# Performance work log

Hardware: AMD Instinct MI355X
Metric: run time of the kernel (lower is better)

The kernel has to match this reference:

```python
import jax, jax.numpy as jnp
import numpy as np

N = 100000
E = 3200000
NEG_SLOPE = 0.2


def _gat(x, W, a_src, a_dst, b, src, dst, n):
    """PyG-style GATConv (eval mode, self-loops already appended to src/dst)."""
    H, C = a_src.shape
    h = (x @ W).reshape(n, H, C)                       # [N,H,C]
    es = jnp.einsum('nhc,hc->nh', h, a_src)            # per-node src logits
    ed = jnp.einsum('nhc,hc->nh', h, a_dst)
    e = jax.nn.leaky_relu(es[src] + ed[dst], NEG_SLOPE)  # [E,H]
    m = jax.ops.segment_max(e, dst, num_segments=n)    # stable softmax per dst
    ee = jnp.exp(e - m[dst])
    z = jax.ops.segment_sum(ee, dst, num_segments=n)
    alpha = ee / z[dst]                                # softmax over in-edges
    out = jax.ops.segment_sum(h[src] * alpha[:, :, None], dst, num_segments=n)
    return out.reshape(n, H * C) + b


def setup_inputs() -> dict:
    key = jax.random.key(0)
    ks = jax.random.split(key, 25)
    rn = lambda k, s, sc=0.1: jax.random.normal(k, s, dtype=jnp.float32) * sc
    return {
        'x1': rn(ks[0], (N, 8), 1.0),
        'x2': rn(ks[1], (N, 10), 1.0),
        'edge_index': jax.random.randint(ks[2], (2, E), 0, N, dtype=jnp.int32),
        'num_nodes': N,
        'Wq': rn(ks[3], (8, 16)), 'bq': rn(ks[4], (16,)),
        'Wk': rn(ks[5], (10, 16)), 'bk': rn(ks[6], (16,)),
        'Wv': rn(ks[7], (18, 16)), 'bv': rn(ks[8], (16,)),
        'W1': rn(ks[9], (16, 32)), 'a1s': rn(ks[10], (8, 4)), 'a1d': rn(ks[11], (8, 4)), 'b1': rn(ks[12], (32,)),
        'W2': rn(ks[13], (32, 16)), 'a2s': rn(ks[14], (4, 4)), 'a2d': rn(ks[15], (4, 4)), 'b2': rn(ks[16], (16,)),
        'W3': rn(ks[17], (16, 8)), 'a3s': rn(ks[18], (2, 4)), 'a3d': rn(ks[19], (2, 4)), 'b3': rn(ks[20], (8,)),
        'Wl2': rn(ks[21], (8, 1)),
    }


def reference(x1, x2, edge_index, num_nodes, Wq, bq, Wk, bk, Wv, bv,
              W1, a1s, a1d, b1, W2, a2s, a2d, b2, W3, a3s, a3d, b3, Wl2):
    n = num_nodes
    q = x1 @ Wq + bq                                   # [N,16]
    k = x2 @ Wk + bk                                   # [N,16]
    v = jnp.concatenate([x1, x2], axis=1) @ Wv + bv    # [N,16]
    score = jnp.sum(q * k, axis=1)                     # bmm(q[:,None,:], k[:,:,None]).squeeze()
    attw = jax.nn.softmax(score)[:, None]              # softmax over all nodes
    fused = attw * v                                   # [N,16]

    sl = jnp.arange(n, dtype=edge_index.dtype)         # GATConv adds self-loops
    src = jnp.concatenate([edge_index[0], sl])
    dst = jnp.concatenate([edge_index[1], sl])

    h1 = _gat(fused, W1, a1s, a1d, b1, src, dst, n)    # [N,32]
    h2 = _gat(h1, W2, a2s, a2d, b2, src, dst, n)       # [N,16]
    x4 = _gat(h2, W3, a3s, a3d, b3, src, dst, n)       # [N,8]; dropout=identity (eval)

    # Row-normalized adjacency (no self loops), expressed as O(E) segment ops.
    r, c = edge_index[0], edge_index[1]
    deg = jax.ops.segment_sum(jnp.ones_like(r, dtype=x4.dtype), r, num_segments=n)
    inv = jnp.where(deg > 0, 1.0 / deg, 0.0)[:, None]
    R3 = jax.ops.segment_sum(x4[c], r, num_segments=n) * inv  # Adj_norm @ x4
    local = jnp.sum(x4 * R3, axis=1, keepdims=True)    # sum_j Adjn[i,j]*(x4_i . x4_j)
    glob = R3 @ Wl2                                    # lin2 (no bias)
    return local + glob                                # [N,1]
```

## Files before the change

kernel.cpp:

```cpp
#include <hip/hip_runtime.h>

#define TPB 256
#define CAP 9216
#define EPB 4096
#define OFSW 784
#define GBPAD 784

typedef float f32x4 __attribute__((ext_vector_type(4)));
typedef float f32x2 __attribute__((ext_vector_type(2)));

__device__ __forceinline__ float lrelu(float x) { return x > 0.f ? x : 0.2f * x; }

__device__ __forceinline__ unsigned bfr(float x) {
  unsigned u = __float_as_uint(x);
  return (u + 0x7FFFu + ((u >> 16) & 1u)) >> 16;
}
__device__ __forceinline__ unsigned pk(float a, float b) { return bfr(a) | (bfr(b) << 16); }
__device__ __forceinline__ float ubf(unsigned us) { return __uint_as_float(us << 16); }

__global__ void __launch_bounds__(TPB) k_bucket(
    const int* __restrict__ ei, int E, int N,
    unsigned* __restrict__ items2, int* __restrict__ ofs)
{
  __shared__ int hist[1024];
  __shared__ int lofs[1024];
  __shared__ int scan_s[TPB];
  __shared__ unsigned stage[2 * EPB];
  int tid = threadIdx.x;
  for (int i = tid; i < 1024; i += TPB) hist[i] = 0;
  int s0 = blockIdx.x * EPB;
  int nE = min(EPB, E - s0);
  int sv[16], dv[16];
  __syncthreads();
#pragma unroll
  for (int k = 0; k < 4; k++) {
    int li = tid * 4 + k * TPB * 4;
    if (li + 3 < nE) {
      int4 s4 = *(const int4*)(ei + s0 + li);
      int4 d4 = *(const int4*)(ei + E + s0 + li);
      sv[k*4+0] = s4.x; sv[k*4+1] = s4.y; sv[k*4+2] = s4.z; sv[k*4+3] = s4.w;
      dv[k*4+0] = d4.x; dv[k*4+1] = d4.y; dv[k*4+2] = d4.z; dv[k*4+3] = d4.w;
#pragma unroll
      for (int j = 0; j < 4; j++) {
        atomicAdd(&hist[dv[k*4+j] >> 8], 1);
        atomicAdd(&hist[(N + sv[k*4+j]) >> 8], 1);
      }
    } else {
      for (int j = 0; j < 4; j++) {
        if (li + j < nE) {
          sv[k*4+j] = ei[s0 + li + j];
          dv[k*4+j] = ei[E + s0 + li + j];
          atomicAdd(&hist[dv[k*4+j] >> 8], 1);
          atomicAdd(&hist[(N + sv[k*4+j]) >> 8], 1);
        }
      }
    }
  }
  __syncthreads();
  int b0 = tid * 4;
  int c0 = hist[b0], c1 = hist[b0 + 1], c2 = hist[b0 + 2], c3 = hist[b0 + 3];
  int tsum = c0 + c1 + c2 + c3;
  scan_s[tid] = tsum;
  __syncthreads();
#pragma unroll
  for (int o = 1; o < TPB; o <<= 1) {
    int t = (tid >= o) ? scan_s[tid - o] : 0;
    __syncthreads();
    scan_s[tid] += t;
    __syncthreads();
  }
  int run = scan_s[tid] - tsum;
  int cs[4] = {c0, c1, c2, c3};
#pragma unroll
  for (int j = 0; j < 4; j++) {
    int b = b0 + j;
    lofs[b] = run;
    hist[b] = 0;
    run += cs[j];
  }
  __syncthreads();
#pragma unroll
  for (int k = 0; k < 16; k++) {
    int li = tid * 4 + (k >> 2) * TPB * 4 + (k & 3);
    if (li < nE) {
      int s = sv[k], d = dv[k];
      int b1 = d >> 8;
      int p1 = lofs[b1] + atomicAdd(&hist[b1], 1);
      stage[p1] = ((unsigned)(d & 255) << 24) | (unsigned)s;
      int k2 = N + s, b2 = k2 >> 8;
      int p2 = lofs[b2] + atomicAdd(&hist[b2], 1);
      stage[p2] = ((unsigned)(k2 & 255) << 24) | (unsigned)d;
    }
  }
  __syncthreads();
  int total = 2 * nE;
  size_t obase = (size_t)blockIdx.x * (2 * EPB);
  for (int idx = tid; idx < total; idx += TPB)
    __builtin_nontemporal_store(stage[idx], items2 + obase + idx);
  int orow = blockIdx.x * OFSW;
  for (int i = tid; i < OFSW; i += TPB)
    ofs[orow + i] = lofs[i];
}

__global__ void __launch_bounds__(TPB) k_t(
    const int* __restrict__ ofs, int* __restrict__ ofsT, int nB)
{
  __shared__ int tile[32][33];
  int lx = threadIdx.x & 31, ly = threadIdx.x >> 5;
  int b0 = blockIdx.y * 32, k0 = blockIdx.x * 32;
#pragma unroll
  for (int r = 0; r < 32; r += 8) {
    int b = b0 + ly + r, k = k0 + lx;
    tile[ly + r][lx] = (b < nB && k < OFSW) ? ofs[b * OFSW + k] : 0;
  }
  __syncthreads();
#pragma unroll
  for (int r = 0; r < 32; r += 8) {
    int k = k0 + ly + r, b = b0 + lx;
    if (k < OFSW && b < GBPAD) ofsT[k * GBPAD + b] = tile[lx][ly + r];
  }
}

__global__ void __launch_bounds__(TPB) k_csr2(
    const int* __restrict__ ofsT, const unsigned* __restrict__ items2, int nB,
    unsigned* __restrict__ items, int* __restrict__ rowptr, int* __restrict__ rowend, int n2)
{
  __shared__ unsigned stage[CAP];
  __shared__ int cnt_s[TPB], scan_s[TPB], off_s[TPB];
  int tid = threadIdx.x, k = blockIdx.x;
  cnt_s[tid] = 0;
  int o0[4], cl[4];
  int tsum = 0;
#pragma unroll
  for (int m = 0; m < 4; m++) {
    int b = tid + m * TPB;
    if (b < nB) {
      int a0 = ofsT[(size_t)k * GBPAD + b];
      int a1 = ofsT[(size_t)(k + 1) * GBPAD + b];
      o0[m] = a0; cl[m] = a1 - a0;
    } else { o0[m] = 0; cl[m] = 0; }
    tsum += cl[m];
  }
  scan_s[tid] = tsum;
  __syncthreads();
#pragma unroll
  for (int o = 1; o < TPB; o <<= 1) {
    int t = (tid >= o) ? scan_s[tid - o] : 0;
    __syncthreads();
    scan_s[tid] += t;
    __syncthreads();
  }
  int cnt = min(scan_s[TPB - 1], CAP);
  int dst = scan_s[tid] - tsum;
#pragma unroll
  for (int m = 0; m < 4; m++) {
    int b = tid + m * TPB;
    const unsigned* src = items2 + (size_t)b * (2 * EPB) + o0[m];
    for (int j = 0; j < cl[m]; j++) {
      int p = dst + j;
      if (p < CAP) stage[p] = src[j];
    }
    dst += cl[m];
  }
  __syncthreads();
  for (int i = tid; i < cnt; i += TPB) atomicAdd(&cnt_s[stage[i] >> 24], 1);
  __syncthreads();
  int v = cnt_s[tid];
  scan_s[tid] = v;
  __syncthreads();
#pragma unroll
  for (int o = 1; o < TPB; o <<= 1) {
    int t = (tid >= o) ? scan_s[tid - o] : 0;
    __syncthreads();
    scan_s[tid] += t;
    __syncthreads();
  }
  int excl = scan_s[tid] - v;
  off_s[tid] = excl;
  size_t bbase = (size_t)k * CAP;
  int g = k * 256 + tid;
  if (g < n2) { rowptr[g] = (int)bbase + excl; rowend[g] = (int)bbase + excl + v; }
  cnt_s[tid] = 0;
  __syncthreads();
  for (int i = tid; i < cnt; i += TPB) {
    unsigned u = stage[i];
    int kk = u >> 24;
    int r = atomicAdd(&cnt_s[kk], 1);
    items[bbase + off_s[kk] + r] = u & 0xFFFFFFu;
  }
}


__global__ void __launch_bounds__(TPB) k_score(
    const float* __restrict__ x1, const float* __restrict__ x2,
    const float* __restrict__ Wq, const float* __restrict__ bq,
    const float* __restrict__ Wk, const float* __restrict__ bk,
    float* __restrict__ escore, float* __restrict__ sumexp, int N)
{
  __shared__ float sWq[128], sWk[160], sbq[16], sbk[16];
  for (int i = threadIdx.x; i < 128; i += TPB) sWq[i] = Wq[i];
  for (int i = threadIdx.x; i < 160; i += TPB) sWk[i] = Wk[i];
  if (threadIdx.x < 16) { sbq[threadIdx.x] = bq[threadIdx.x]; sbk[threadIdx.x] = bk[threadIdx.x]; }
  __syncthreads();
  int n = blockIdx.x * TPB + threadIdx.x;
  float e = 0.f;
  if (n < N) {
    float a[8], b[10];
#pragma unroll
    for (int i = 0; i < 8; i++) a[i] = x1[n*8 + i];
#pragma unroll
    for (int i = 0; i < 10; i++) b[i] = x2[n*10 + i];
    float score = 0.f;
#pragma unroll
    for (int j = 0; j < 16; j++) {
      float q = sbq[j], k = sbk[j];
#pragma unroll
      for (int i = 0; i < 8; i++) q += a[i] * sWq[i*16 + j];
#pragma unroll
      for (int i = 0; i < 10; i++) k += b[i] * sWk[i*16 + j];
      score += q * k;
    }
    e = __expf(score);
    escore[n] = e;
  }
  float v = e;
#pragma unroll
  for (int off = 32; off > 0; off >>= 1) v += __shfl_down(v, off);
  __shared__ float red[TPB / 64];
  if ((threadIdx.x & 63) == 0) red[threadIdx.x >> 6] = v;
  __syncthreads();
  if (threadIdx.x == 0) {
    float s = 0.f;
#pragma unroll
    for (int w = 0; w < TPB / 64; w++) s += red[w];
    atomicAdd(sumexp, s);
  }
}

__global__ void __launch_bounds__(TPB) k_A1(
    const float* __restrict__ x1, const float* __restrict__ x2,
    const float* __restrict__ Wv, const float* __restrict__ bv,
    const float* __restrict__ W1, const float* __restrict__ a1s, const float* __restrict__ a1d,
    const float* __restrict__ escore, const float* __restrict__ sumexp,
    unsigned* __restrict__ rec1a, unsigned* __restrict__ rec1b,
    float* __restrict__ ed, int N)
{
  __shared__ float sWv[288], sbv[16], sW1[512], sas[32], sad[32];
  for (int i = threadIdx.x; i < 288; i += TPB) sWv[i] = Wv[i];
  for (int i = threadIdx.x; i < 512; i += TPB) sW1[i] = W1[i];
  if (threadIdx.x < 16) sbv[threadIdx.x] = bv[threadIdx.x];
  if (threadIdx.x < 32) { sas[threadIdx.x] = a1s[threadIdx.x]; sad[threadIdx.x] = a1d[threadIdx.x]; }
  __syncthreads();
  int n = blockIdx.x * TPB + threadIdx.x;
  if (n >= N) return;
  float w = escore[n] / sumexp[0];
  float f[16];
  {
    float a[8], b[10];
#pragma unroll
    for (int i = 0; i < 8; i++) a[i] = x1[n*8 + i];
#pragma unroll
    for (int i = 0; i < 10; i++) b[i] = x2[n*10 + i];
#pragma unroll
    for (int j = 0; j < 16; j++) {
      float v = sbv[j];
#pragma unroll
      for (int i = 0; i < 8; i++) v += a[i] * sWv[i*16 + j];
#pragma unroll
      for (int i = 0; i < 10; i++) v += b[i] * sWv[(8 + i)*16 + j];
      f[j] = w * v;
    }
  }
  float hr[32], esv[8], edv[8];
#pragma unroll
  for (int j = 0; j < 32; j++) {
    float s = 0.f;
#pragma unroll
    for (int i = 0; i < 16; i++) s += f[i] * sW1[i*32 + j];
    hr[j] = s;
  }
#pragma unroll
  for (int hh = 0; hh < 8; hh++) {
    float s = 0.f, d = 0.f;
#pragma unroll
    for (int c = 0; c < 4; c++) { s += hr[hh*4+c]*sas[hh*4+c]; d += hr[hh*4+c]*sad[hh*4+c]; }
    esv[hh] = s; edv[hh] = d;
  }
  unsigned* ra = rec1a + (size_t)n*10;
  unsigned* rb = rec1b + (size_t)n*10;
  ra[0] = pk(esv[0], esv[1]); ra[1] = pk(esv[2], esv[3]);
  rb[0] = pk(esv[4], esv[5]); rb[1] = pk(esv[6], esv[7]);
#pragma unroll
  for (int hh = 0; hh < 4; hh++) {
    ra[2+2*hh] = pk(hr[hh*4+0], hr[hh*4+1]);
    ra[3+2*hh] = pk(hr[hh*4+2], hr[hh*4+3]);
    rb[2+2*hh] = pk(hr[16+hh*4+0], hr[16+hh*4+1]);
    rb[3+2*hh] = pk(hr[16+hh*4+2], hr[16+hh*4+3]);
  }
  f32x4 e0 = {edv[0], edv[1], edv[2], edv[3]};
  f32x4 e1 = {edv[4], edv[5], edv[6], edv[7]};
  *(f32x4*)(ed + n*8)     = e0;
  *(f32x4*)(ed + n*8 + 4) = e1;
}

__global__ void __launch_bounds__(TPB) k_B2(
    const float* __restrict__ W2, const float* __restrict__ a2s, const float* __restrict__ a2d,
    const float* __restrict__ X,
    unsigned* __restrict__ rec2, float* __restrict__ ed, int N)
{
  __shared__ float sW[512], sas[16], sad[16];
  for (int i = threadIdx.x; i < 512; i += TPB) sW[i] = W2[i];
  if (threadIdx.x < 16) { sas[threadIdx.x] = a2s[threadIdx.x]; sad[threadIdx.x] = a2d[threadIdx.x]; }
  __syncthreads();
  int n = blockIdx.x * TPB + threadIdx.x;
  if (n >= N) return;
  float Xr[32];
#pragma unroll
  for (int i = 0; i < 8; i++) {
    f32x4 t = __builtin_nontemporal_load((const f32x4*)(X + n*32) + i);
    Xr[i*4+0] = t.x; Xr[i*4+1] = t.y; Xr[i*4+2] = t.z; Xr[i*4+3] = t.w;
  }
  float hr[16];
#pragma unroll
  for (int j = 0; j < 16; j++) {
    float s = 0.f;
#pragma unroll
    for (int f = 0; f < 32; f++) s += Xr[f] * sW[f*16 + j];
    hr[j] = s;
  }
  float esv[4], edv[4];
#pragma unroll
  for (int hh = 0; hh < 4; hh++) {
    float s = 0.f, d = 0.f;
#pragma unroll
    for (int c = 0; c < 4; c++) { s += hr[hh*4+c]*sas[hh*4+c]; d += hr[hh*4+c]*sad[hh*4+c]; }
    esv[hh] = s; edv[hh] = d;
  }
  unsigned* r = rec2 + (size_t)n*10;
  r[0] = pk(esv[0], esv[1]); r[1] = pk(esv[2], esv[3]);
#pragma unroll
  for (int hh = 0; hh < 4; hh++) {
    r[2+2*hh] = pk(hr[hh*4+0], hr[hh*4+1]);
    r[3+2*hh] = pk(hr[hh*4+2], hr[hh*4+3]);
  }
  f32x4 e0 = {edv[0], edv[1], edv[2], edv[3]};
  *(f32x4*)(ed + n*8) = e0;
}

__global__ void __launch_bounds__(TPB) k_B3(
    const float* __restrict__ W3, const float* __restrict__ a3s, const float* __restrict__ a3d,
    const float* __restrict__ X3,
    float* __restrict__ rec3, float* __restrict__ ed, int N)
{
  __shared__ float sW[128], sas[8], sad[8];
  for (int i = threadIdx.x; i < 128; i += TPB) sW[i] = W3[i];
  if (threadIdx.x < 8) { sas[threadIdx.x] = a3s[threadIdx.x]; sad[threadIdx.x] = a3d[threadIdx.x]; }
  __syncthreads();
  int n = blockIdx.x * TPB + threadIdx.x;
  if (n >= N) return;
  float Xr[16];
#pragma unroll
  for (int i = 0; i < 4; i++) {
    f32x4 t = __builtin_nontemporal_load((const f32x4*)(X3 + n*16) + i);
    Xr[i*4+0] = t.x; Xr[i*4+1] = t.y; Xr[i*4+2] = t.z; Xr[i*4+3] = t.w;
  }
  float hr[8];
#pragma unroll
  for (int j = 0; j < 8; j++) {
    float s = 0.f;
#pragma unroll
    for (int f = 0; f < 16; f++) s += Xr[f] * sW[f*8 + j];
    hr[j] = s;
  }
  float* r = rec3 + (size_t)n*10;
#pragma unroll
  for (int hh = 0; hh < 2; hh++) {
    float s = 0.f, d = 0.f;
#pragma unroll
    for (int c = 0; c < 4; c++) { s += hr[hh*4+c]*sas[hh*4+c]; d += hr[hh*4+c]*sad[hh*4+c]; }
    r[hh] = s;
    ed[n*8 + hh] = d;
  }
#pragma unroll
  for (int hh = 0; hh < 2; hh++) {
    f32x2 a = {hr[hh*4+0], hr[hh*4+1]};
    f32x2 b = {hr[hh*4+2], hr[hh*4+3]};
    *(f32x2*)(r + 2 + hh*4)     = a;
    *(f32x2*)(r + 2 + hh*4 + 2) = b;
  }
}

template<int OS, int HOFF>
__global__ void __launch_bounds__(TPB) k_gat4(
    const int* __restrict__ rowptr, const int* __restrict__ rowend, const int* __restrict__ col,
    const unsigned* __restrict__ rec, const float* __restrict__ ed,
    const float* __restrict__ bias, float* __restrict__ out, int N)
{
  int wave = (blockIdx.x * TPB + threadIdx.x) >> 6;
  if (wave >= N) return;
  int lane = threadIdx.x & 63;
  int hh = lane & 3, j = lane >> 2;
  int d = wave;
  int e0 = rowptr[d], deg = rowend[d] - e0;
  float edv = ed[d*8 + HOFF + hh];
  float z = 0.f;
  f32x4 acc = {0.f, 0.f, 0.f, 0.f};
  for (int t = j; t <= deg; t += 16) {
    int s = (t == deg) ? d : __builtin_nontemporal_load(col + e0 + t);
    const unsigned* rp = rec + (size_t)s*10;
    unsigned ew = rp[hh >> 1];
    uint2 hv = *(const uint2*)(rp + 2 + 2*hh);
    float esv = ubf((ew >> ((hh & 1) * 16)) & 0xFFFFu);
    float w = __expf(lrelu(esv + edv));
    z += w;
    acc.x += w * ubf(hv.x & 0xFFFFu); acc.y += w * ubf(hv.x >> 16);
    acc.z += w * ubf(hv.y & 0xFFFFu); acc.w += w * ubf(hv.y >> 16);
  }
#pragma unroll
  for (int m = 4; m < 64; m <<= 1) {
    z += __shfl_xor(z, m);
    acc.x += __shfl_xor(acc.x, m); acc.y += __shfl_xor(acc.y, m);
    acc.z += __shfl_xor(acc.z, m); acc.w += __shfl_xor(acc.w, m);
  }
  if (j == 0) {
    float inv = 1.f / z;
    const f32x4 bb = *(const f32x4*)(bias + (HOFF + hh)*4);
    f32x4 o = { acc.x*inv + bb.x, acc.y*inv + bb.y, acc.z*inv + bb.z, acc.w*inv + bb.w };
    __builtin_nontemporal_store(o, (f32x4*)(out + (size_t)d*OS + (HOFF + hh)*4));
  }
}

__global__ void __launch_bounds__(TPB) k_gat3(
    const int* __restrict__ rowptr, const int* __restrict__ rowend, const int* __restrict__ col,
    const float* __restrict__ rec, const float* __restrict__ ed,
    const float* __restrict__ b3, float* __restrict__ x4, int N)
{
  int wave = (blockIdx.x * TPB + threadIdx.x) >> 6;
  if (wave >= N) return;
  int lane = threadIdx.x & 63;
  int hh = lane & 1, j = lane >> 1;
  int d = wave;
  int e0 = rowptr[d], deg = rowend[d] - e0;
  float edv = ed[d*8 + hh];
  float z = 0.f;
  f32x4 acc = {0.f, 0.f, 0.f, 0.f};
  for (int t = j; t <= deg; t += 32) {
    int s = (t == deg) ? d : __builtin_nontemporal_load(col + e0 + t);
    const float* rp = rec + (size_t)s*10;
    float esv = rp[hh];
    f32x2 a = *(const f32x2*)(rp + 2 + hh*4);
    f32x2 b = *(const f32x2*)(rp + 2 + hh*4 + 2);
    float w = __expf(lrelu(esv + edv));
    z += w; acc.x += w*a.x; acc.y += w*a.y; acc.z += w*b.x; acc.w += w*b.y;
  }
#pragma unroll
  for (int m = 2; m < 64; m <<= 1) {
    z += __shfl_xor(z, m);
    acc.x += __shfl_xor(acc.x, m); acc.y += __shfl_xor(acc.y, m);
    acc.z += __shfl_xor(acc.z, m); acc.w += __shfl_xor(acc.w, m);
  }
  if (j == 0) {
    float inv = 1.f / z;
    const f32x4 bb = *(const f32x4*)(b3 + hh*4);
    f32x4 o = { acc.x*inv + bb.x, acc.y*inv + bb.y, acc.z*inv + bb.z, acc.w*inv + bb.w };
    __builtin_nontemporal_store(o, (f32x4*)(x4 + d*8 + hh*4));
  }
}

__global__ void __launch_bounds__(TPB) k_adj_final(
    const int* __restrict__ rowptr, const int* __restrict__ rowend, const int* __restrict__ col,
    const float* __restrict__ x4, const float* __restrict__ Wl2,
    float* __restrict__ out, int N)
{
  __shared__ float sW[8];
  if (threadIdx.x < 8) sW[threadIdx.x] = Wl2[threadIdx.x];
  __syncthreads();
  int wave = (blockIdx.x * TPB + threadIdx.x) >> 6;
  if (wave >= N) return;
  int lane = threadIdx.x & 63;
  int q = lane & 1, j = lane >> 1;
  int r = wave;
  int e0 = rowptr[N + r], deg = rowend[N + r] - e0;
  f32x4 acc = {0.f, 0.f, 0.f, 0.f};
  for (int t = j; t < deg; t += 32) {
    int c = __builtin_nontemporal_load(col + e0 + t);
    f32x4 xv = *(const f32x4*)(x4 + c*8 + q*4);
    acc.x += xv.x; acc.y += xv.y; acc.z += xv.z; acc.w += xv.w;
  }
#pragma unroll
  for (int m = 2; m < 64; m <<= 1) {
    acc.x += __shfl_xor(acc.x, m); acc.y += __shfl_xor(acc.y, m);
    acc.z += __shfl_xor(acc.z, m); acc.w += __shfl_xor(acc.w, m);
  }
  float part = 0.f;
  if (j == 0) {
    float inv = deg > 0 ? 1.f / (float)deg : 0.f;
    f32x4 R = { acc.x*inv, acc.y*inv, acc.z*inv, acc.w*inv };
    f32x4 xo = *(const f32x4*)(x4 + r*8 + q*4);
    part = xo.x*R.x + xo.y*R.y + xo.z*R.z + xo.w*R.w
         + R.x*sW[q*4+0] + R.y*sW[q*4+1] + R.z*sW[q*4+2] + R.w*sW[q*4+3];
  }
  part += __shfl_xor(part, 1);
  if (lane == 0) out[r] = part;
}

extern "C" void kernel_launch(void* const* d_in, const int* in_sizes, int n_in,
                              void* d_out, int out_size, void* d_ws, size_t ws_size,
                              hipStream_t stream)
{
  const float* x1  = (const float*)d_in[0];
  const float* x2  = (const float*)d_in[1];
  const int*   ei  = (const int*)d_in[2];
  const float* Wq  = (const float*)d_in[4];
  const float* bq  = (const float*)d_in[5];
  const float* Wk  = (const float*)d_in[6];
  const float* bk  = (const float*)d_in[7];
  const float* Wv  = (const float*)d_in[8];
  const float* bv  = (const float*)d_in[9];
  const float* W1  = (const float*)d_in[10];
  const float* a1s = (const float*)d_in[11];
  const float* a1d = (const float*)d_in[12];
  const float* b1  = (const float*)d_in[13];
  const float* W2  = (const float*)d_in[14];
  const float* a2s = (const float*)d_in[15];
  const float* a2d = (const float*)d_in[16];
  const float* b2  = (const float*)d_in[17];
  const float* W3  = (const float*)d_in[18];
  const float* a3s = (const float*)d_in[19];
  const float* a3d = (const float*)d_in[20];
  const float* b3  = (const float*)d_in[21];
  const float* Wl2 = (const float*)d_in[22];

  int N = in_sizes[0] / 8;
  int E = in_sizes[2] / 2;
  int n2 = 2 * N;
  int NB = (n2 + 255) >> 8;
  int gB = (E + EPB - 1) / EPB;

  float* sumexp = (float*)d_ws;
  int* rowptr   = (int*)(sumexp + 16);
  int* rowend   = rowptr + (size_t)n2;
  unsigned* itemsCSR = (unsigned*)(rowend + (size_t)n2);
  unsigned* regionA  = itemsCSR + (size_t)NB * CAP;
  unsigned* items2 = regionA;
  int* ofs  = (int*)(items2 + (size_t)gB * (2 * EPB));
  int* ofsT = ofs + (size_t)gB * OFSW;
  size_t raSize = (size_t)gB * (2 * EPB + OFSW) + (size_t)OFSW * GBPAD;
  unsigned* rec1a = regionA;
  unsigned* rec1b = rec1a + 10ull*N;
  unsigned* rec2  = rec1b + 10ull*N;
  float* rec3     = (float*)(rec2 + 10ull*N);
  float* ed       = rec3 + 10ull*N;
  float* escore   = ed + 8ull*N;
  float* X        = (float*)(regionA + raSize);
  float* X3 = X;
  float* x4 = (float*)rec1b;

  int gN = (N + TPB - 1) / TPB;
  int g64 = (int)(((long long)N * 64 + TPB - 1) / TPB);

  (void)hipMemsetAsync(sumexp, 0, 16 * sizeof(float), stream);

  k_bucket<<<gB, TPB, 0, stream>>>(ei, E, N, items2, ofs);
  dim3 gt((OFSW + 31) / 32, (gB + 31) / 32);
  k_t<<<gt, TPB, 0, stream>>>(ofs, ofsT, gB);
  k_csr2<<<NB, TPB, 0, stream>>>(ofsT, items2, gB, itemsCSR, rowptr, rowend, n2);
  int* colv = (int*)itemsCSR;

  k_score<<<gN, TPB, 0, stream>>>(x1, x2, Wq, bq, Wk, bk, escore, sumexp, N);
  k_A1<<<gN, TPB, 0, stream>>>(x1, x2, Wv, bv, W1, a1s, a1d, escore, sumexp, rec1a, rec1b, ed, N);

  k_gat4<32, 0><<<g64, TPB, 0, stream>>>(rowptr, rowend, colv, rec1a, ed, b1, X, N);
  k_gat4<32, 4><<<g64, TPB, 0, stream>>>(rowptr, rowend, colv, rec1b, ed, b1, X, N);
  k_B2<<<gN, TPB, 0, stream>>>(W2, a2s, a2d, X, rec2, ed, N);
  k_gat4<16, 0><<<g64, TPB, 0, stream>>>(rowptr, rowend, colv, rec2, ed, b2, X3, N);
  k_B3<<<gN, TPB, 0, stream>>>(W3, a3s, a3d, X3, rec3, ed, N);
  k_gat3<<<g64, TPB, 0, stream>>>(rowptr, rowend, colv, rec3, ed, b3, x4, N);

  k_adj_final<<<g64, TPB, 0, stream>>>(rowptr, rowend, colv, x4, Wl2, (float*)d_out, N);
}
```

Measured before the change: 495.5 us.

## Repack per-node GAT records into 16-byte per-head slots for single vector gathers

Changes the per-node source records of all three GAT layers so each head's logit (now fp32) and its four bf16-packed features sit in one aligned 16-byte slot. Each edge gather then needs a single 128-bit load instead of several scalar or 8-byte loads at unaligned offsets. Layer 3 features drop from fp32 to bf16. The CSR staging copy is also vectorized with aligned 4-wide loads. In exchange the records grow (16 words per node instead of 10, with padding), which adds write and gather footprint, and layer 3 loses feature precision.

```diff
diff --git a/kernel.cpp b/kernel.cpp
--- a/kernel.cpp
+++ b/kernel.cpp
@@ -8,6 +8,7 @@
 
 typedef float f32x4 __attribute__((ext_vector_type(4)));
 typedef float f32x2 __attribute__((ext_vector_type(2)));
+typedef unsigned u32x4 __attribute__((ext_vector_type(4)));
 
 __device__ __forceinline__ float lrelu(float x) { return x > 0.f ? x : 0.2f * x; }
 
@@ -156,11 +157,24 @@
   for (int m = 0; m < 4; m++) {
     int b = tid + m * TPB;
     const unsigned* src = items2 + (size_t)b * (2 * EPB) + o0[m];
-    for (int j = 0; j < cl[m]; j++) {
+    int c = cl[m];
+    int j = 0;
+    int head = (4 - (o0[m] & 3)) & 3; if (head > c) head = c;
+    for (; j < head; j++) { int p = dst + j; if (p < CAP) stage[p] = src[j]; }
+    for (; j + 3 < c; j += 4) {
+      u32x4 v = *(const u32x4*)(src + j);
       int p = dst + j;
-      if (p < CAP) stage[p] = src[j];
+      if (p + 3 < CAP) {
+        stage[p] = v.x; stage[p+1] = v.y; stage[p+2] = v.z; stage[p+3] = v.w;
+      } else {
+        if (p < CAP) stage[p] = v.x;
+        if (p+1 < CAP) stage[p+1] = v.y;
+        if (p+2 < CAP) stage[p+2] = v.z;
+        if (p+3 < CAP) stage[p+3] = v.w;
+      }
     }
-    dst += cl[m];
+    for (; j < c; j++) { int p = dst + j; if (p < CAP) stage[p] = src[j]; }
+    dst += c;
   }
   __syncthreads();
   for (int i = tid; i < cnt; i += TPB) atomicAdd(&cnt_s[stage[i] >> 24], 1);
@@ -286,16 +300,16 @@
     for (int c = 0; c < 4; c++) { s += hr[hh*4+c]*sas[hh*4+c]; d += hr[hh*4+c]*sad[hh*4+c]; }
     esv[hh] = s; edv[hh] = d;
   }
-  unsigned* ra = rec1a + (size_t)n*10;
-  unsigned* rb = rec1b + (size_t)n*10;
-  ra[0] = pk(esv[0], esv[1]); ra[1] = pk(esv[2], esv[3]);
-  rb[0] = pk(esv[4], esv[5]); rb[1] = pk(esv[6], esv[7]);
+  unsigned* ra = rec1a + (size_t)n*16;
+  unsigned* rb = rec1b + (size_t)n*16;
 #pragma unroll
   for (int hh = 0; hh < 4; hh++) {
-    ra[2+2*hh] = pk(hr[hh*4+0], hr[hh*4+1]);
-    ra[3+2*hh] = pk(hr[hh*4+2], hr[hh*4+3]);
-    rb[2+2*hh] = pk(hr[16+hh*4+0], hr[16+hh*4+1]);
-    rb[3+2*hh] = pk(hr[16+hh*4+2], hr[16+hh*4+3]);
+    u32x4 qa = { __float_as_uint(esv[hh]),
+                 pk(hr[hh*4+0], hr[hh*4+1]), pk(hr[hh*4+2], hr[hh*4+3]), 0u };
+    u32x4 qb = { __float_as_uint(esv[4+hh]),
+                 pk(hr[16+hh*4+0], hr[16+hh*4+1]), pk(hr[16+hh*4+2], hr[16+hh*4+3]), 0u };
+    __builtin_nontemporal_store(qa, (u32x4*)(ra + hh*4));
+    __builtin_nontemporal_store(qb, (u32x4*)(rb + hh*4));
   }
   f32x4 e0 = {edv[0], edv[1], edv[2], edv[3]};
   f32x4 e1 = {edv[4], edv[5], edv[6], edv[7]};
@@ -328,29 +342,23 @@
     for (int f = 0; f < 32; f++) s += Xr[f] * sW[f*16 + j];
     hr[j] = s;
   }
-  float esv[4], edv[4];
+  unsigned* r = rec2 + (size_t)n*16;
 #pragma unroll
   for (int hh = 0; hh < 4; hh++) {
     float s = 0.f, d = 0.f;
 #pragma unroll
     for (int c = 0; c < 4; c++) { s += hr[hh*4+c]*sas[hh*4+c]; d += hr[hh*4+c]*sad[hh*4+c]; }
-    esv[hh] = s; edv[hh] = d;
-  }
-  unsigned* r = rec2 + (size_t)n*10;
-  r[0] = pk(esv[0], esv[1]); r[1] = pk(esv[2], esv[3]);
-#pragma unroll
-  for (int hh = 0; hh < 4; hh++) {
-    r[2+2*hh] = pk(hr[hh*4+0], hr[hh*4+1]);
-    r[3+2*hh] = pk(hr[hh*4+2], hr[hh*4+3]);
-  }
-  f32x4 e0 = {edv[0], edv[1], edv[2], edv[3]};
-  *(f32x4*)(ed + n*8) = e0;
+    u32x4 q = { __float_as_uint(s),
+                pk(hr[hh*4+0], hr[hh*4+1]), pk(hr[hh*4+2], hr[hh*4+3]), 0u };
+    __builtin_nontemporal_store(q, (u32x4*)(r + hh*4));
+    ed[n*8 + hh] = d;
+  }
 }
 
 __global__ void __launch_bounds__(TPB) k_B3(
     const float* __restrict__ W3, const float* __restrict__ a3s, const float* __restrict__ a3d,
     const float* __restrict__ X3,
-    float* __restrict__ rec3, float* __restrict__ ed, int N)
+    unsigned* __restrict__ rec3, float* __restrict__ ed, int N)
 {
   __shared__ float sW[128], sas[8], sad[8];
   for (int i = threadIdx.x; i < 128; i += TPB) sW[i] = W3[i];
@@ -372,21 +380,16 @@
     for (int f = 0; f < 16; f++) s += Xr[f] * sW[f*8 + j];
     hr[j] = s;
   }
-  float* r = rec3 + (size_t)n*10;
+  unsigned* r = rec3 + (size_t)n*8;
 #pragma unroll
   for (int hh = 0; hh < 2; hh++) {
     float s = 0.f, d = 0.f;
 #pragma unroll
     for (int c = 0; c < 4; c++) { s += hr[hh*4+c]*sas[hh*4+c]; d += hr[hh*4+c]*sad[hh*4+c]; }
-    r[hh] = s;
+    u32x4 q = { __float_as_uint(s),
+                pk(hr[hh*4+0], hr[hh*4+1]), pk(hr[hh*4+2], hr[hh*4+3]), 0u };
+    __builtin_nontemporal_store(q, (u32x4*)(r + hh*4));
     ed[n*8 + hh] = d;
-  }
-#pragma unroll
-  for (int hh = 0; hh < 2; hh++) {
-    f32x2 a = {hr[hh*4+0], hr[hh*4+1]};
-    f32x2 b = {hr[hh*4+2], hr[hh*4+3]};
-    *(f32x2*)(r + 2 + hh*4)     = a;
-    *(f32x2*)(r + 2 + hh*4 + 2) = b;
   }
 }
 
@@ -407,14 +410,11 @@
   f32x4 acc = {0.f, 0.f, 0.f, 0.f};
   for (int t = j; t <= deg; t += 16) {
     int s = (t == deg) ? d : __builtin_nontemporal_load(col + e0 + t);
-    const unsigned* rp = rec + (size_t)s*10;
-    unsigned ew = rp[hh >> 1];
-    uint2 hv = *(const uint2*)(rp + 2 + 2*hh);
-    float esv = ubf((ew >> ((hh & 1) * 16)) & 0xFFFFu);
-    float w = __expf(lrelu(esv + edv));
+    u32x4 q = *(const u32x4*)(rec + (size_t)s*16 + hh*4);
+    float w = __expf(lrelu(__uint_as_float(q.x) + edv));
     z += w;
-    acc.x += w * ubf(hv.x & 0xFFFFu); acc.y += w * ubf(hv.x >> 16);
-    acc.z += w * ubf(hv.y & 0xFFFFu); acc.w += w * ubf(hv.y >> 16);
+    acc.x += w * ubf(q.y & 0xFFFFu); acc.y += w * ubf(q.y >> 16);
+    acc.z += w * ubf(q.z & 0xFFFFu); acc.w += w * ubf(q.z >> 16);
   }
 #pragma unroll
   for (int m = 4; m < 64; m <<= 1) {
@@ -432,7 +432,7 @@
 
 __global__ void __launch_bounds__(TPB) k_gat3(
     const int* __restrict__ rowptr, const int* __restrict__ rowend, const int* __restrict__ col,
-    const float* __restrict__ rec, const float* __restrict__ ed,
+    const unsigned* __restrict__ rec, const float* __restrict__ ed,
     const float* __restrict__ b3, float* __restrict__ x4, int N)
 {
   int wave = (blockIdx.x * TPB + threadIdx.x) >> 6;
@@ -446,12 +446,11 @@
   f32x4 acc = {0.f, 0.f, 0.f, 0.f};
   for (int t = j; t <= deg; t += 32) {
     int s = (t == deg) ? d : __builtin_nontemporal_load(col + e0 + t);
-    const float* rp = rec + (size_t)s*10;
-    float esv = rp[hh];
-    f32x2 a = *(const f32x2*)(rp + 2 + hh*4);
-    f32x2 b = *(const f32x2*)(rp + 2 + hh*4 + 2);
-    float w = __expf(lrelu(esv + edv));
-    z += w; acc.x += w*a.x; acc.y += w*a.y; acc.z += w*b.x; acc.w += w*b.y;
+    u32x4 q = *(const u32x4*)(rec + (size_t)s*8 + hh*4);
+    float w = __expf(lrelu(__uint_as_float(q.x) + edv));
+    z += w;
+    acc.x += w * ubf(q.y & 0xFFFFu); acc.y += w * ubf(q.y >> 16);
+    acc.z += w * ubf(q.z & 0xFFFFu); acc.w += w * ubf(q.z >> 16);
   }
 #pragma unroll
   for (int m = 2; m < 64; m <<= 1) {
@@ -547,10 +546,10 @@
   int* ofsT = ofs + (size_t)gB * OFSW;
   size_t raSize = (size_t)gB * (2 * EPB + OFSW) + (size_t)OFSW * GBPAD;
   unsigned* rec1a = regionA;
-  unsigned* rec1b = rec1a + 10ull*N;
-  unsigned* rec2  = rec1b + 10ull*N;
-  float* rec3     = (float*)(rec2 + 10ull*N);
-  float* ed       = rec3 + 10ull*N;
+  unsigned* rec1b = rec1a + 16ull*N;
+  unsigned* rec2  = rec1b + 16ull*N;
+  unsigned* rec3  = rec2 + 16ull*N;
+  float* ed       = (float*)(rec3 + 8ull*N);
   float* escore   = ed + 8ull*N;
   float* X        = (float*)(regionA + raSize);
   float* X3 = X;
```

Result: faster. 482.8 us (-2.6%).
